# Kernel optimization log

Measured on AMD Instinct MI355X. Metric: run time of the kernel, lower is better.

The kernel has to match this reference:

```python
import jax, jax.numpy as jnp
import numpy as np

HIDDEN = 2048
HEADS = 16
HEAD_DIM = HIDDEN // HEADS


def setup_inputs() -> dict:
    key = jax.random.key(0)
    kx, kq, kk, kv, ko = jax.random.split(key, 5)
    s = 1.0 / np.sqrt(HIDDEN)
    return {
        "x": jax.random.normal(kx, (2, 2048, HIDDEN), dtype=jnp.float32),
        "Wq": jax.random.normal(kq, (HIDDEN, HIDDEN), dtype=jnp.float32) * s,
        "Wk": jax.random.normal(kk, (HIDDEN, HIDDEN), dtype=jnp.float32) * s,
        "Wv": jax.random.normal(kv, (HIDDEN, HIDDEN), dtype=jnp.float32) * s,
        "Wo": jax.random.normal(ko, (HIDDEN, HIDDEN), dtype=jnp.float32) * s,
    }


def reference(x, Wq, Wk, Wv, Wo):
    B, S, H = x.shape
    nh, hd = HEADS, HEAD_DIM
    # projections (nn.Linear: y = x @ W.T; here W stored as [in, out] so x @ W)
    q = (x @ Wq).reshape(B, S, nh, hd).transpose(0, 2, 1, 3)  # [B,nh,S,hd]
    k = (x @ Wk).reshape(B, S, nh, hd).transpose(0, 2, 1, 3)
    v = (x @ Wv).reshape(B, S, nh, hd).transpose(0, 2, 1, 3)
    scores = jnp.einsum("bhqd,bhkd->bhqk", q, k) / jnp.sqrt(jnp.float32(hd))
    causal = jnp.tril(jnp.ones((S, S), dtype=bool))  # keep lower triangle
    scores = jnp.where(causal, scores, jnp.finfo(scores.dtype).min)
    attn = jax.nn.softmax(scores, axis=-1)
    out = jnp.einsum("bhqk,bhkd->bhqd", attn, v)
    out = out.transpose(0, 2, 1, 3).reshape(B, S, H)
    return out @ Wo
```

## Files before the change

### kernel.cpp

```cpp
#include <hip/hip_runtime.h>
#include <stdint.h>

typedef unsigned short u16;
typedef __bf16 bf16x8 __attribute__((ext_vector_type(8)));
typedef short s4 __attribute__((ext_vector_type(4)));
typedef float f32x4 __attribute__((ext_vector_type(4)));

#define B_ 2
#define S_ 2048
#define H_ 2048
#define NH_ 16
#define HD_ 128

#define SL2f (0.08838834764831845f * 1.4426950408889634f)

__device__ __forceinline__ u16 f2bf(float f) {
    uint32_t u = __float_as_uint(f);
    u += 0x7fff + ((u >> 16) & 1);
    return (u16)(u >> 16);
}

__device__ __forceinline__ uint32_t pk_bf16(float lo, float hi) {
    return __builtin_amdgcn_perm(__float_as_uint(hi), __float_as_uint(lo), 0x07060302u);
}

__device__ __forceinline__ void gl_lds16(const u16* g, u16* l) {
    __builtin_amdgcn_global_load_lds(
        (const __attribute__((address_space(1))) void*)g,
        (__attribute__((address_space(3))) void*)l, 16, 0, 0);
}

union U2S4 { uint2 u; s4 s; };

__global__ __launch_bounds__(256) void prep_kernel(
        const float* __restrict__ x,
        const float* __restrict__ w0, const float* __restrict__ w1,
        const float* __restrict__ w2, const float* __restrict__ w3,
        u16* __restrict__ xb, u16* __restrict__ dqkv, u16* __restrict__ dwo) {
    int z = blockIdx.z;
    int tx = threadIdx.x, ty = threadIdx.y;
    if (z == 4) {
        int tid = ty * 32 + tx;
        size_t base = ((size_t)(blockIdx.y * 64 + blockIdx.x)) * 2048 + tid * 8;
#pragma unroll
        for (int i = 0; i < 2; i++) {
            float4 v = *(const float4*)&x[base + i * 4];
            ushort4 o;
            o.x = f2bf(v.x); o.y = f2bf(v.y); o.z = f2bf(v.z); o.w = f2bf(v.w);
            *(ushort4*)&xb[base + i * 4] = o;
        }
        return;
    }
    const float* src = (z == 0) ? w0 : (z == 1) ? w1 : (z == 2) ? w2 : w3;
    u16* dst = (z < 3) ? (dqkv + (size_t)z * H_ * H_) : dwo;
    __shared__ float tile[32][33];
    int n0 = blockIdx.x * 32, k0 = blockIdx.y * 32;
#pragma unroll
    for (int i = 0; i < 4; i++)
        tile[ty + i * 8][tx] = src[(size_t)(k0 + ty + i * 8) * H_ + n0 + tx];
    __syncthreads();
#pragma unroll
    for (int i = 0; i < 4; i++)
        dst[(size_t)(n0 + ty + i * 8) * H_ + k0 + tx] = f2bf(tile[tx][ty + i * 8]);
}

template <int MODE>
__global__ __launch_bounds__(512, 2) void gemm_bt(
        const u16* __restrict__ A, const u16* __restrict__ Bt, float* __restrict__ Cout,
        u16* __restrict__ q, u16* __restrict__ k, u16* __restrict__ v,
        int M, int N, int K) {
    __shared__ u16 sm[65536];
    int tid = threadIdx.x;
    int w = tid >> 6, lane = tid & 63, quad = lane >> 4, l16 = lane & 15;
    int wm = w >> 2, wn = w & 3;
    int m0 = blockIdx.y * 128, n0 = blockIdx.x * 256;
    const int NT = K >> 6;

    f32x4 acc[4][4];
#pragma unroll
    for (int mi = 0; mi < 4; mi++)
#pragma unroll
        for (int ni = 0; ni < 4; ni++)
            acc[mi][ni] = (f32x4){0.f, 0.f, 0.f, 0.f};

    auto stageA = [&](int kt) {
        const u16* ga = A + (size_t)m0 * K + kt * 64;
        u16* As = sm + (kt & 1) * 8192;
#pragma unroll
        for (int j = 0; j < 2; j++) {
            int p = j * 512 + tid;
            int row = p >> 3, c = (p & 7) ^ (row & 7);
            gl_lds16(&ga[(size_t)row * K + c * 8], &As[(j * 512 + w * 64) * 8]);
        }
    };
    auto stageB = [&](int kt) {
        const u16* gb = Bt + (size_t)n0 * K + kt * 64;
        u16* Bs = sm + 16384 + (kt % 3) * 16384;
#pragma unroll
        for (int j = 0; j < 4; j++) {
            int p = j * 512 + tid;
            int row = p >> 3, c = (p & 7) ^ (row & 7);
            gl_lds16(&gb[(size_t)row * K + c * 8], &Bs[(j * 512 + w * 64) * 8]);
        }
    };

    stageA(0);
    stageB(0);
    stageB(1);

    for (int kt = 0; kt < NT; kt++) {
        __builtin_amdgcn_sched_barrier(0);
        if (kt == NT - 1)
            asm volatile("s_waitcnt vmcnt(0) lgkmcnt(0)" ::: "memory");
        else
            asm volatile("s_waitcnt vmcnt(4) lgkmcnt(0)" ::: "memory");
        __builtin_amdgcn_s_barrier();
        __builtin_amdgcn_sched_barrier(0);

        if (kt + 1 < NT) stageA(kt + 1);
        if (kt + 2 < NT) stageB(kt + 2);

        const u16* As = sm + (kt & 1) * 8192;
        const u16* Bs = sm + 16384 + (kt % 3) * 16384;
#pragma unroll
        for (int ks = 0; ks < 2; ks++) {
            bf16x8 af[4], bfr[4];
#pragma unroll
            for (int mi = 0; mi < 4; mi++) {
                int row = wm * 64 + mi * 16 + l16;
                af[mi] = *(const bf16x8*)&As[row * 64 + (((ks * 4 + quad) ^ (row & 7)) * 8)];
            }
#pragma unroll
            for (int ni = 0; ni < 4; ni++) {
                int row = wn * 64 + ni * 16 + l16;
                bfr[ni] = *(const bf16x8*)&Bs[row * 64 + (((ks * 4 + quad) ^ (row & 7)) * 8)];
            }
#pragma unroll
            for (int mi = 0; mi < 4; mi++)
#pragma unroll
                for (int ni = 0; ni < 4; ni++)
                    acc[mi][ni] = __builtin_amdgcn_mfma_f32_16x16x32_bf16(af[mi], bfr[ni], acc[mi][ni], 0, 0, 0);
        }
    }

    if (MODE == 0 && n0 >= 4096) {
        __syncthreads();
#pragma unroll
        for (int mi = 0; mi < 4; mi++) {
#pragma unroll
            for (int ni = 0; ni < 4; ni++) {
                int nl = wn * 64 + ni * 16 + l16;
#pragma unroll
                for (int r = 0; r < 4; r++) {
                    int ml = wm * 64 + mi * 16 + quad * 4 + r;
                    sm[nl * 128 + (((ml >> 3) ^ (nl & 15)) * 8) + (ml & 7)] = f2bf(acc[mi][ni][r]);
                }
            }
        }
        __syncthreads();
        int b = m0 >> 11, s0 = m0 & 2047;
#pragma unroll
        for (int i = 0; i < 8; i++) {
            int cu = tid + i * 512;
            int nl = cu >> 4, mc = cu & 15;
            int4 val = *(const int4*)&sm[nl * 128 + ((mc ^ (nl & 15)) * 8)];
            int ngl = (n0 - 4096) + nl;
            int h = ngl >> 7, d = ngl & 127;
            *(int4*)&v[((size_t)((b * NH_ + h) * HD_ + d)) * S_ + s0 + mc * 8] = val;
        }
    } else {
#pragma unroll
        for (int mi = 0; mi < 4; mi++) {
#pragma unroll
            for (int ni = 0; ni < 4; ni++) {
                int ng = n0 + wn * 64 + ni * 16 + l16;
#pragma unroll
                for (int r = 0; r < 4; r++) {
                    int mg = m0 + wm * 64 + mi * 16 + quad * 4 + r;
                    float val = acc[mi][ni][r];
                    if (MODE == 0) {
                        int which = ng >> 11;
                        int rem = ng & 2047;
                        int h = rem >> 7, d = rem & 127;
                        int b = mg >> 11, s = mg & 2047;
                        if (which == 0)
                            q[((size_t)((b * NH_ + h) * S_ + s)) * HD_ + d] = f2bf(val * SL2f);
                        else
                            k[((size_t)((b * NH_ + h) * S_ + s)) * HD_ + d] = f2bf(val);
                    } else {
                        Cout[(size_t)mg * N + ng] = val;
                    }
                }
            }
        }
    }
}

__global__ __launch_bounds__(256, 2) void flash_kernel(
        const u16* __restrict__ Q, const u16* __restrict__ Kb,
        const u16* __restrict__ VT, u16* __restrict__ Ctx) {
    __shared__ u16 Ks[2][64 * 128];
    __shared__ u16 Vs[2][128 * 64];
    int tid = threadIdx.x;
    int w = tid >> 6, lane = tid & 63, quad = lane >> 4, l16 = lane & 15;

    int id = blockIdx.x;
    int bh = id & 31;
    int b = bh >> 4, h = bh & 15;
    int pair = id >> 5;
    int qts = pair, qtl = 31 - pair;
    int n0 = qts + 1;

    size_t bhoff = ((size_t)b * NH_ + h) * S_ * HD_;
    const u16* Qp = Q + bhoff;
    const u16* Kp = Kb + bhoff;
    const u16* Vp = VT + bhoff;

    auto stageK = [&](int t, int buf) {
        int kv0 = ((t >= n0) ? (t - n0) : t) * 64;
#pragma unroll
        for (int j = 0; j < 4; j++) {
            int base = (j * 4 + w) * 64;
            int p = base + lane;
            int row = p >> 4;
            int c = (p & 15) ^ (row & 15);
            gl_lds16(&Kp[(size_t)(kv0 + row) * HD_ + c * 8], &Ks[buf][base * 8]);
        }
    };
    auto stageV = [&](int t, int buf) {
        int kv0 = ((t >= n0) ? (t - n0) : t) * 64;
#pragma unroll
        for (int j = 0; j < 4; j++) {
            int base = (j * 4 + w) * 64;
            int p = base + lane;
            int row = p >> 3;
            int c = (p & 7) ^ (row & 7);
            gl_lds16(&Vp[(size_t)row * S_ + kv0 + c * 8], &Vs[buf][base * 8]);
        }
    };

    int q0 = qts * 64;
    int qg = q0 + w * 16 + l16;
    bf16x8 qf[4];
#pragma unroll
    for (int ks = 0; ks < 4; ks++)
        qf[ks] = *(const bf16x8*)&Qp[(size_t)qg * HD_ + ks * 32 + quad * 8];

    float l_part = 0.f;
    f32x4 ao[8];
#pragma unroll
    for (int dt = 0; dt < 8; dt++) ao[dt] = (f32x4){0.f, 0.f, 0.f, 0.f};

    auto epilogue = [&]() {
        float l = l_part;
        l += __shfl_xor(l, 16);
        l += __shfl_xor(l, 32);
        float inv = 1.0f / l;
        size_t base = ((size_t)b * S_ + qg) * H_ + h * HD_;
#pragma unroll
        for (int dt = 0; dt < 8; dt++) {
            u16 o0 = f2bf(ao[dt][0] * inv), o1 = f2bf(ao[dt][1] * inv);
            u16 o2 = f2bf(ao[dt][2] * inv), o3 = f2bf(ao[dt][3] * inv);
            uint2 st;
            st.x = (uint32_t)o0 | ((uint32_t)o1 << 16);
            st.y = (uint32_t)o2 | ((uint32_t)o3 << 16);
            *(uint2*)&Ctx[base + dt * 16 + quad * 4] = st;
        }
    };

    stageK(0, 0);
    stageV(0, 0);

    for (int t = 0; t < 33; t++) {
        if (t == n0) {
            epilogue();
            q0 = qtl * 64;
            qg = q0 + w * 16 + l16;
#pragma unroll
            for (int ks = 0; ks < 4; ks++)
                qf[ks] = *(const bf16x8*)&Qp[(size_t)qg * HD_ + ks * 32 + quad * 8];
            l_part = 0.f;
#pragma unroll
            for (int dt = 0; dt < 8; dt++) ao[dt] = (f32x4){0.f, 0.f, 0.f, 0.f};
        }
        int buf = t & 1;
        __syncthreads();

        f32x4 sc[4];
#pragma unroll
        for (int nt = 0; nt < 4; nt++) {
            sc[nt] = (f32x4){0.f, 0.f, 0.f, 0.f};
            int row = nt * 16 + l16;
#pragma unroll
            for (int ks = 0; ks < 4; ks++) {
                bf16x8 kf = *(const bf16x8*)&Ks[buf][row * 128 + (((ks * 4 + quad) ^ (row & 15)) * 8)];
                sc[nt] = __builtin_amdgcn_mfma_f32_16x16x32_bf16(kf, qf[ks], sc[nt], 0, 0, 0);
            }
        }

        __syncthreads();

        if (t + 1 < 33) {
            stageK(t + 1, buf ^ 1);
            stageV(t + 1, buf ^ 1);
        }

        bool diag = (t == n0 - 1) || (t == 32);
        U2S4 pk[4];
        if (!diag) {
#pragma unroll
            for (int nt = 0; nt < 4; nt++) {
                float p0 = exp2f(sc[nt][0]), p1 = exp2f(sc[nt][1]);
                float p2 = exp2f(sc[nt][2]), p3 = exp2f(sc[nt][3]);
                l_part += (p0 + p1) + (p2 + p3);
                pk[nt].u.x = pk_bf16(p0, p1);
                pk[nt].u.y = pk_bf16(p2, p3);
            }
        } else {
            int kvb = q0 + quad * 4;
#pragma unroll
            for (int nt = 0; nt < 4; nt++) {
                int kv = kvb + nt * 16;
                float p0 = (kv + 0 > qg) ? 0.f : exp2f(sc[nt][0]);
                float p1 = (kv + 1 > qg) ? 0.f : exp2f(sc[nt][1]);
                float p2 = (kv + 2 > qg) ? 0.f : exp2f(sc[nt][2]);
                float p3 = (kv + 3 > qg) ? 0.f : exp2f(sc[nt][3]);
                l_part += (p0 + p1) + (p2 + p3);
                pk[nt].u.x = pk_bf16(p0, p1);
                pk[nt].u.y = pk_bf16(p2, p3);
            }
        }

#pragma unroll
        for (int kt = 0; kt < 4; kt++) {
#pragma unroll
            for (int dt = 0; dt < 8; dt++) {
                int d = dt * 16 + l16;
                int c = kt * 2 + (quad >> 1);
                s4 va = *(const s4*)&Vs[buf][d * 64 + ((c ^ (d & 7)) * 8) + (quad & 1) * 4];
                ao[dt] = __builtin_amdgcn_mfma_f32_16x16x16bf16_1k(va, pk[kt].s, ao[dt], 0, 0, 0);
            }
        }
    }
    epilogue();
}

extern "C" void kernel_launch(void* const* d_in, const int* in_sizes, int n_in,
                              void* d_out, int out_size, void* d_ws, size_t ws_size,
                              hipStream_t stream) {
    const float* x  = (const float*)d_in[0];
    const float* Wq = (const float*)d_in[1];
    const float* Wk = (const float*)d_in[2];
    const float* Wv = (const float*)d_in[3];
    const float* Wo = (const float*)d_in[4];
    float* out = (float*)d_out;

    const size_t MB = 1024 * 1024;
    char* ws = (char*)d_ws;
    u16* Xb    = (u16*)(ws);
    u16* WqkvT = (u16*)(ws + 16 * MB);
    u16* WoT   = (u16*)(ws + 40 * MB);
    u16* Qb    = (u16*)(ws + 48 * MB);
    u16* Kbuf  = (u16*)(ws + 64 * MB);
    u16* VT    = (u16*)(ws + 80 * MB);
    u16* Ctx   = (u16*)(ws + 96 * MB);

    prep_kernel<<<dim3(64, 64, 5), dim3(32, 8), 0, stream>>>(x, Wq, Wk, Wv, Wo, Xb, WqkvT, WoT);
    gemm_bt<0><<<dim3(24, 32), 512, 0, stream>>>(Xb, WqkvT, nullptr, Qb, Kbuf, VT, 4096, 6144, 2048);
    flash_kernel<<<512, 256, 0, stream>>>(Qb, Kbuf, VT, Ctx);
    gemm_bt<1><<<dim3(8, 32), 512, 0, stream>>>(Ctx, WoT, out, nullptr, nullptr, nullptr, 4096, 2048, 2048);
}
```

Measured before the change: 352.6 us.

## Split QKV GEMM into half-tile pipeline phases and add separate output GEMM

The QKV projection GEMM drops from triple-buffered B to double buffering. Each k-step is split into two halves: the next A or B tile is issued, then half the MFMAs run at raised wave priority between barriers. This aims to overlap global-to-LDS loads with compute using less LDS. The output projection moves to a new 256-thread, 128x128-tile kernel with a simple load-sync-compute loop and no prefetch. That doubles the block count for the smaller GEMM but serializes its loads with compute.

```diff
diff --git a/kernel.cpp b/kernel.cpp
--- a/kernel.cpp
+++ b/kernel.cpp
@@ -28,6 +28,19 @@
     __builtin_amdgcn_global_load_lds(
         (const __attribute__((address_space(1))) void*)g,
         (__attribute__((address_space(3))) void*)l, 16, 0, 0);
+}
+
+__device__ __forceinline__ void sync_vm2() {
+    __builtin_amdgcn_sched_barrier(0);
+    asm volatile("s_waitcnt vmcnt(2)" ::: "memory");
+    __builtin_amdgcn_s_barrier();
+    __builtin_amdgcn_sched_barrier(0);
+}
+__device__ __forceinline__ void sync_vm0() {
+    __builtin_amdgcn_sched_barrier(0);
+    asm volatile("s_waitcnt vmcnt(0)" ::: "memory");
+    __builtin_amdgcn_s_barrier();
+    __builtin_amdgcn_sched_barrier(0);
 }
 
 union U2S4 { uint2 u; s4 s; };
@@ -64,12 +77,11 @@
         dst[(size_t)(n0 + ty + i * 8) * H_ + k0 + tx] = f2bf(tile[tx][ty + i * 8]);
 }
 
-template <int MODE>
-__global__ __launch_bounds__(512, 2) void gemm_bt(
-        const u16* __restrict__ A, const u16* __restrict__ Bt, float* __restrict__ Cout,
+__global__ __launch_bounds__(512, 2) void gemm_qkv(
+        const u16* __restrict__ A, const u16* __restrict__ Bt,
         u16* __restrict__ q, u16* __restrict__ k, u16* __restrict__ v,
         int M, int N, int K) {
-    __shared__ u16 sm[65536];
+    __shared__ u16 sm[49152];
     int tid = threadIdx.x;
     int w = tid >> 6, lane = tid & 63, quad = lane >> 4, l16 = lane & 15;
     int wm = w >> 2, wn = w & 3;
@@ -95,7 +107,7 @@
     };
     auto stageB = [&](int kt) {
         const u16* gb = Bt + (size_t)n0 * K + kt * 64;
-        u16* Bs = sm + 16384 + (kt % 3) * 16384;
+        u16* Bs = sm + 16384 + (kt & 1) * 16384;
 #pragma unroll
         for (int j = 0; j < 4; j++) {
             int p = j * 512 + tid;
@@ -106,50 +118,68 @@
 
     stageA(0);
     stageB(0);
-    stageB(1);
+    sync_vm2();
 
     for (int kt = 0; kt < NT; kt++) {
-        __builtin_amdgcn_sched_barrier(0);
-        if (kt == NT - 1)
-            asm volatile("s_waitcnt vmcnt(0) lgkmcnt(0)" ::: "memory");
-        else
-            asm volatile("s_waitcnt vmcnt(4) lgkmcnt(0)" ::: "memory");
-        __builtin_amdgcn_s_barrier();
-        __builtin_amdgcn_sched_barrier(0);
-
-        if (kt + 1 < NT) stageA(kt + 1);
-        if (kt + 2 < NT) stageB(kt + 2);
-
-        const u16* As = sm + (kt & 1) * 8192;
-        const u16* Bs = sm + 16384 + (kt % 3) * 16384;
-#pragma unroll
-        for (int ks = 0; ks < 2; ks++) {
-            bf16x8 af[4], bfr[4];
+        bool lastT = (kt == NT - 1);
+        const u16* Ab = sm + (kt & 1) * 8192;
+        const u16* Bb = sm + 16384 + (kt & 1) * 16384;
+
+        bf16x8 af[2][4], bfl[2][2];
+#pragma unroll
+        for (int ks = 0; ks < 2; ks++)
 #pragma unroll
             for (int mi = 0; mi < 4; mi++) {
                 int row = wm * 64 + mi * 16 + l16;
-                af[mi] = *(const bf16x8*)&As[row * 64 + (((ks * 4 + quad) ^ (row & 7)) * 8)];
-            }
+                af[ks][mi] = *(const bf16x8*)&Ab[row * 64 + (((ks * 4 + quad) ^ (row & 7)) * 8)];
+            }
+#pragma unroll
+        for (int ks = 0; ks < 2; ks++)
+#pragma unroll
+            for (int ni = 0; ni < 2; ni++) {
+                int row = wn * 32 + ni * 16 + l16;
+                bfl[ks][ni] = *(const bf16x8*)&Bb[row * 64 + (((ks * 4 + quad) ^ (row & 7)) * 8)];
+            }
+        if (!lastT) stageA(kt + 1);
+        __builtin_amdgcn_s_setprio(1);
+#pragma unroll
+        for (int ks = 0; ks < 2; ks++)
+#pragma unroll
+            for (int mi = 0; mi < 4; mi++)
+#pragma unroll
+                for (int ni = 0; ni < 2; ni++)
+                    acc[mi][ni] = __builtin_amdgcn_mfma_f32_16x16x32_bf16(af[ks][mi], bfl[ks][ni], acc[mi][ni], 0, 0, 0);
+        __builtin_amdgcn_s_setprio(0);
+        if (!lastT) sync_vm2();
+        else sync_vm0();
+
+        bf16x8 bfh[2][2];
+#pragma unroll
+        for (int ks = 0; ks < 2; ks++)
+#pragma unroll
+            for (int ni = 0; ni < 2; ni++) {
+                int row = 128 + wn * 32 + ni * 16 + l16;
+                bfh[ks][ni] = *(const bf16x8*)&Bb[row * 64 + (((ks * 4 + quad) ^ (row & 7)) * 8)];
+            }
+        if (!lastT) stageB(kt + 1);
+        __builtin_amdgcn_s_setprio(1);
+#pragma unroll
+        for (int ks = 0; ks < 2; ks++)
+#pragma unroll
+            for (int mi = 0; mi < 4; mi++)
+#pragma unroll
+                for (int ni = 0; ni < 2; ni++)
+                    acc[mi][ni + 2] = __builtin_amdgcn_mfma_f32_16x16x32_bf16(af[ks][mi], bfh[ks][ni], acc[mi][ni + 2], 0, 0, 0);
+        __builtin_amdgcn_s_setprio(0);
+        if (!lastT) sync_vm2();
+    }
+
+    if (n0 >= 4096) {
+#pragma unroll
+        for (int mi = 0; mi < 4; mi++) {
 #pragma unroll
             for (int ni = 0; ni < 4; ni++) {
-                int row = wn * 64 + ni * 16 + l16;
-                bfr[ni] = *(const bf16x8*)&Bs[row * 64 + (((ks * 4 + quad) ^ (row & 7)) * 8)];
-            }
-#pragma unroll
-            for (int mi = 0; mi < 4; mi++)
-#pragma unroll
-                for (int ni = 0; ni < 4; ni++)
-                    acc[mi][ni] = __builtin_amdgcn_mfma_f32_16x16x32_bf16(af[mi], bfr[ni], acc[mi][ni], 0, 0, 0);
-        }
-    }
-
-    if (MODE == 0 && n0 >= 4096) {
-        __syncthreads();
-#pragma unroll
-        for (int mi = 0; mi < 4; mi++) {
-#pragma unroll
-            for (int ni = 0; ni < 4; ni++) {
-                int nl = wn * 64 + ni * 16 + l16;
+                int nl = (ni >> 1) * 128 + wn * 32 + (ni & 1) * 16 + l16;
 #pragma unroll
                 for (int r = 0; r < 4; r++) {
                     int ml = wm * 64 + mi * 16 + quad * 4 + r;
@@ -173,24 +203,87 @@
         for (int mi = 0; mi < 4; mi++) {
 #pragma unroll
             for (int ni = 0; ni < 4; ni++) {
-                int ng = n0 + wn * 64 + ni * 16 + l16;
+                int ng = n0 + (ni >> 1) * 128 + wn * 32 + (ni & 1) * 16 + l16;
+                int which = ng >> 11;
+                int rem = ng & 2047;
+                int h = rem >> 7, d = rem & 127;
 #pragma unroll
                 for (int r = 0; r < 4; r++) {
                     int mg = m0 + wm * 64 + mi * 16 + quad * 4 + r;
                     float val = acc[mi][ni][r];
-                    if (MODE == 0) {
-                        int which = ng >> 11;
-                        int rem = ng & 2047;
-                        int h = rem >> 7, d = rem & 127;
-                        int b = mg >> 11, s = mg & 2047;
-                        if (which == 0)
-                            q[((size_t)((b * NH_ + h) * S_ + s)) * HD_ + d] = f2bf(val * SL2f);
-                        else
-                            k[((size_t)((b * NH_ + h) * S_ + s)) * HD_ + d] = f2bf(val);
-                    } else {
-                        Cout[(size_t)mg * N + ng] = val;
-                    }
+                    int b = mg >> 11, s = mg & 2047;
+                    if (which == 0)
+                        q[((size_t)((b * NH_ + h) * S_ + s)) * HD_ + d] = f2bf(val * SL2f);
+                    else
+                        k[((size_t)((b * NH_ + h) * S_ + s)) * HD_ + d] = f2bf(val);
                 }
+            }
+        }
+    }
+}
+
+__global__ __launch_bounds__(256, 2) void gemm_out(
+        const u16* __restrict__ A, const u16* __restrict__ Bt, float* __restrict__ Cout,
+        int M, int N, int K) {
+    __shared__ u16 sm[2 * 128 * 64];
+    u16* As = sm;
+    u16* Bs = sm + 128 * 64;
+    int tid = threadIdx.x;
+    int w = tid >> 6, lane = tid & 63, quad = lane >> 4, l16 = lane & 15;
+    int wm = w >> 1, wn = w & 1;
+    int m0 = blockIdx.y * 128, n0 = blockIdx.x * 128;
+
+    f32x4 acc[4][4];
+#pragma unroll
+    for (int mi = 0; mi < 4; mi++)
+#pragma unroll
+        for (int ni = 0; ni < 4; ni++)
+            acc[mi][ni] = (f32x4){0.f, 0.f, 0.f, 0.f};
+
+    for (int k0 = 0; k0 < K; k0 += 64) {
+        const u16* ga = A + (size_t)m0 * K + k0;
+        const u16* gb = Bt + (size_t)n0 * K + k0;
+#pragma unroll
+        for (int j = 0; j < 4; j++) {
+            int base = (j * 4 + w) * 64;
+            int p = base + lane;
+            int row = p >> 3;
+            int c = (p & 7) ^ (row & 7);
+            gl_lds16(&ga[(size_t)row * K + c * 8], &As[base * 8]);
+            gl_lds16(&gb[(size_t)row * K + c * 8], &Bs[base * 8]);
+        }
+        __syncthreads();
+#pragma unroll
+        for (int ks = 0; ks < 2; ks++) {
+            bf16x8 af[4], bfr[4];
+#pragma unroll
+            for (int mi = 0; mi < 4; mi++) {
+                int row = wm * 64 + mi * 16 + l16;
+                af[mi] = *(const bf16x8*)&As[row * 64 + (((ks * 4 + quad) ^ (row & 7)) * 8)];
+            }
+#pragma unroll
+            for (int ni = 0; ni < 4; ni++) {
+                int row = wn * 64 + ni * 16 + l16;
+                bfr[ni] = *(const bf16x8*)&Bs[row * 64 + (((ks * 4 + quad) ^ (row & 7)) * 8)];
+            }
+#pragma unroll
+            for (int mi = 0; mi < 4; mi++)
+#pragma unroll
+                for (int ni = 0; ni < 4; ni++)
+                    acc[mi][ni] = __builtin_amdgcn_mfma_f32_16x16x32_bf16(af[mi], bfr[ni], acc[mi][ni], 0, 0, 0);
+        }
+        __syncthreads();
+    }
+
+#pragma unroll
+    for (int mi = 0; mi < 4; mi++) {
+#pragma unroll
+        for (int ni = 0; ni < 4; ni++) {
+            int ng = n0 + wn * 64 + ni * 16 + l16;
+#pragma unroll
+            for (int r = 0; r < 4; r++) {
+                int mg = m0 + wm * 64 + mi * 16 + quad * 4 + r;
+                Cout[(size_t)mg * N + ng] = acc[mi][ni][r];
             }
         }
     }
@@ -366,7 +459,7 @@
     u16* Ctx   = (u16*)(ws + 96 * MB);
 
     prep_kernel<<<dim3(64, 64, 5), dim3(32, 8), 0, stream>>>(x, Wq, Wk, Wv, Wo, Xb, WqkvT, WoT);
-    gemm_bt<0><<<dim3(24, 32), 512, 0, stream>>>(Xb, WqkvT, nullptr, Qb, Kbuf, VT, 4096, 6144, 2048);
+    gemm_qkv<<<dim3(24, 32), 512, 0, stream>>>(Xb, WqkvT, Qb, Kbuf, VT, 4096, 6144, 2048);
     flash_kernel<<<512, 256, 0, stream>>>(Qb, Kbuf, VT, Ctx);
-    gemm_bt<1><<<dim3(8, 32), 512, 0, stream>>>(Ctx, WoT, out, nullptr, nullptr, nullptr, 4096, 2048, 2048);
-}
+    gemm_out<<<dim3(16, 32), 256, 0, stream>>>(Ctx, WoT, out, 4096, 2048, 2048);
+}
```

Measured after the change: 342.7 us. -2.8%, faster.
